# Performance work log

Hardware: AMD Instinct MI355X
Metric: run time of the kernel (lower is better)

Reference implementation:

```python
import jax, jax.numpy as jnp
import numpy as np

NUM_LINKS = 4096
BUDGET = 100.0      # total_power_budget
PMAX = 0.1          # per_link_max
N_BISECT = 60       # bisection iterations (fp32 converges well before this)


def setup_inputs() -> dict:
    key = jax.random.key(0)
    raw_power = jax.random.normal(key, (8192, NUM_LINKS), dtype=jnp.float32)
    return {"raw_power": raw_power}


def _project(raw):
    """Euclidean projection of each row of raw onto {p : 0<=p<=PMAX, sum(p)<=BUDGET}.

    Closed-form water-filling: if clip(raw,0,PMAX) is feasible it is the answer;
    otherwise p = clip(raw - tau, 0, PMAX) with tau chosen so sum(p) = BUDGET
    (found by batched bisection + one implicit-function Newton correction,
    which also gives the exact QP-projection Jacobian).
    """
    clipped = jnp.clip(raw, 0.0, PMAX)
    feasible = jnp.sum(clipped, axis=-1, keepdims=True) <= BUDGET  # (B,1)

    raw_sg = jax.lax.stop_gradient(raw)
    lo = jnp.min(raw_sg, axis=-1, keepdims=True) - PMAX  # g(lo) = n*PMAX >= BUDGET
    hi = jnp.max(raw_sg, axis=-1, keepdims=True)         # g(hi) = 0

    def body(_, lohi):
        lo, hi = lohi
        mid = 0.5 * (lo + hi)
        g = jnp.sum(jnp.clip(raw_sg - mid, 0.0, PMAX), axis=-1, keepdims=True)
        too_big = g > BUDGET  # tau must increase
        return (jnp.where(too_big, mid, lo), jnp.where(too_big, hi, mid))

    lo, hi = jax.lax.fori_loop(0, N_BISECT, body, (lo, hi))
    tau0 = 0.5 * (lo + hi)  # (B,1), no gradient

    # Implicit-function (Newton) correction: g(tau) = sum(clip(raw-tau,0,PMAX)) = BUDGET.
    # dg/dtau = -n_active, dg/draw_i = active_i  => dtau/draw_i = active_i / n_active.
    active = (raw_sg - tau0 > 0.0) & (raw_sg - tau0 < PMAX)
    n_active = jnp.maximum(jnp.sum(active, axis=-1, keepdims=True).astype(raw.dtype), 1.0)
    g0 = jnp.sum(jnp.clip(raw - tau0, 0.0, PMAX), axis=-1, keepdims=True)
    tau = tau0 + (g0 - BUDGET) / n_active  # value ~= tau0, correct gradient

    p_budget = jnp.clip(raw - tau, 0.0, PMAX)
    return jnp.where(feasible, clipped, p_budget)


def reference(raw_power) -> jnp.ndarray:
    return _project(raw_power)
```

## Files before the change

kernel.cpp:

```cpp
#include <hip/hip_runtime.h>

#define NLINKS 4096
#define VEC 16

constexpr float kPmax = 0.1f;
constexpr float kBudget = 100.0f;
constexpr int kBisect = 20;

__device__ __forceinline__ float waveReduceSum(float x) {
#pragma unroll
  for (int m = 32; m >= 1; m >>= 1) x += __shfl_xor(x, m, 64);
  return x;
}
__device__ __forceinline__ float waveReduceMin(float x) {
#pragma unroll
  for (int m = 32; m >= 1; m >>= 1) x = fminf(x, __shfl_xor(x, m, 64));
  return x;
}
__device__ __forceinline__ float waveReduceMax(float x) {
#pragma unroll
  for (int m = 32; m >= 1; m >>= 1) x = fmaxf(x, __shfl_xor(x, m, 64));
  return x;
}

__device__ __forceinline__ float clip01(float x) {
  return fminf(fmaxf(x, 0.0f), kPmax);
}

__global__ __launch_bounds__(256, 4) void proj_kernel(
    const float* __restrict__ raw, float* __restrict__ out, int rows) {
  const int wave = threadIdx.x >> 6;
  const int lane = threadIdx.x & 63;
  const int row = blockIdx.x * 4 + wave;
  if (row >= rows) return;

  const float4* rp = (const float4*)(raw + (size_t)row * NLINKS);
  float4* op = (float4*)(out + (size_t)row * NLINKS);

  float4 v[VEC];
#pragma unroll
  for (int j = 0; j < VEC; ++j) v[j] = rp[lane + 64 * j];

  float mn = 1e30f, mx = -1e30f;
  float fs0 = 0.f, fs1 = 0.f, fs2 = 0.f, fs3 = 0.f;
#pragma unroll
  for (int j = 0; j < VEC; ++j) {
    mn = fminf(mn, fminf(fminf(v[j].x, v[j].y), fminf(v[j].z, v[j].w)));
    mx = fmaxf(mx, fmaxf(fmaxf(v[j].x, v[j].y), fmaxf(v[j].z, v[j].w)));
    fs0 += clip01(v[j].x);
    fs1 += clip01(v[j].y);
    fs2 += clip01(v[j].z);
    fs3 += clip01(v[j].w);
  }
  const float fs = waveReduceSum((fs0 + fs1) + (fs2 + fs3));
  mn = waveReduceMin(mn);
  mx = waveReduceMax(mx);

  if (fs <= kBudget) {
#pragma unroll
    for (int j = 0; j < VEC; ++j) {
      float4 o;
      o.x = clip01(v[j].x);
      o.y = clip01(v[j].y);
      o.z = clip01(v[j].z);
      o.w = clip01(v[j].w);
      op[lane + 64 * j] = o;
    }
    return;
  }

  float lo = mn - kPmax, hi = mx;
#pragma unroll 1
  for (int it = 0; it < kBisect; ++it) {
    const float mid = 0.5f * (lo + hi);
    float s0 = 0.f, s1 = 0.f, s2 = 0.f, s3 = 0.f;
#pragma unroll
    for (int j = 0; j < VEC; ++j) {
      s0 += clip01(v[j].x - mid);
      s1 += clip01(v[j].y - mid);
      s2 += clip01(v[j].z - mid);
      s3 += clip01(v[j].w - mid);
    }
    const float g = waveReduceSum((s0 + s1) + (s2 + s3));
    const bool big = g > kBudget;
    lo = big ? mid : lo;
    hi = big ? hi : mid;
  }
  const float tau0 = 0.5f * (lo + hi);

  float g0 = 0.f, g1 = 0.f, g2 = 0.f, g3 = 0.f;
  float n0 = 0.f, n1 = 0.f, n2 = 0.f, n3 = 0.f;
#pragma unroll
  for (int j = 0; j < VEC; ++j) {
    float t;
    t = v[j].x - tau0; g0 += clip01(t); n0 += (t > 0.f && t < kPmax) ? 1.f : 0.f;
    t = v[j].y - tau0; g1 += clip01(t); n1 += (t > 0.f && t < kPmax) ? 1.f : 0.f;
    t = v[j].z - tau0; g2 += clip01(t); n2 += (t > 0.f && t < kPmax) ? 1.f : 0.f;
    t = v[j].w - tau0; g3 += clip01(t); n3 += (t > 0.f && t < kPmax) ? 1.f : 0.f;
  }
  const float g = waveReduceSum((g0 + g1) + (g2 + g3));
  float na = waveReduceSum((n0 + n1) + (n2 + n3));
  na = fmaxf(na, 1.0f);
  const float tau = tau0 + (g - kBudget) / na;

#pragma unroll
  for (int j = 0; j < VEC; ++j) {
    float4 o;
    o.x = clip01(v[j].x - tau);
    o.y = clip01(v[j].y - tau);
    o.z = clip01(v[j].z - tau);
    o.w = clip01(v[j].w - tau);
    op[lane + 64 * j] = o;
  }
}

extern "C" void kernel_launch(void* const* d_in, const int* in_sizes, int n_in,
                              void* d_out, int out_size, void* d_ws, size_t ws_size,
                              hipStream_t stream) {
  const float* raw = (const float*)d_in[0];
  float* out = (float*)d_out;
  const int rows = in_sizes[0] / NLINKS;
  const int blocks = (rows + 3) / 4;
  hipLaunchKernelGGL(proj_kernel, dim3(blocks), dim3(256), 0, stream,
                     raw, out, rows);
}
```

Before: 264.0 us.

## Replace bisection with Illinois regula falsi root finder and nontemporal memory ops

Swaps the 20-step bisection for the threshold tau with a 10-step Illinois-style regula falsi bracketed on [0, max], dropping the row-min reduction. Clipping now uses the fmed3 builtin, and the loads and stores go through nontemporal builtins. This halves the number of per-row sweeps over registers and wave reductions. The risk is slower or less accurate convergence for some rows, which the final Newton correction may not fully repair.

```diff
diff --git a/kernel.cpp b/kernel.cpp
--- a/kernel.cpp
+++ b/kernel.cpp
@@ -3,18 +3,15 @@
 #define NLINKS 4096
 #define VEC 16
 
+typedef float fvec4 __attribute__((ext_vector_type(4)));
+
 constexpr float kPmax = 0.1f;
 constexpr float kBudget = 100.0f;
-constexpr int kBisect = 20;
+constexpr int kSecant = 10;
 
 __device__ __forceinline__ float waveReduceSum(float x) {
 #pragma unroll
   for (int m = 32; m >= 1; m >>= 1) x += __shfl_xor(x, m, 64);
-  return x;
-}
-__device__ __forceinline__ float waveReduceMin(float x) {
-#pragma unroll
-  for (int m = 32; m >= 1; m >>= 1) x = fminf(x, __shfl_xor(x, m, 64));
   return x;
 }
 __device__ __forceinline__ float waveReduceMax(float x) {
@@ -24,7 +21,7 @@
 }
 
 __device__ __forceinline__ float clip01(float x) {
-  return fminf(fmaxf(x, 0.0f), kPmax);
+  return __builtin_amdgcn_fmed3f(x, 0.0f, kPmax);
 }
 
 __global__ __launch_bounds__(256, 4) void proj_kernel(
@@ -34,18 +31,17 @@
   const int row = blockIdx.x * 4 + wave;
   if (row >= rows) return;
 
-  const float4* rp = (const float4*)(raw + (size_t)row * NLINKS);
-  float4* op = (float4*)(out + (size_t)row * NLINKS);
+  const fvec4* rp = (const fvec4*)(raw + (size_t)row * NLINKS);
+  fvec4* op = (fvec4*)(out + (size_t)row * NLINKS);
 
-  float4 v[VEC];
+  fvec4 v[VEC];
 #pragma unroll
-  for (int j = 0; j < VEC; ++j) v[j] = rp[lane + 64 * j];
+  for (int j = 0; j < VEC; ++j) v[j] = __builtin_nontemporal_load(&rp[lane + 64 * j]);
 
-  float mn = 1e30f, mx = -1e30f;
+  float mx = -1e30f;
   float fs0 = 0.f, fs1 = 0.f, fs2 = 0.f, fs3 = 0.f;
 #pragma unroll
   for (int j = 0; j < VEC; ++j) {
-    mn = fminf(mn, fminf(fminf(v[j].x, v[j].y), fminf(v[j].z, v[j].w)));
     mx = fmaxf(mx, fmaxf(fmaxf(v[j].x, v[j].y), fmaxf(v[j].z, v[j].w)));
     fs0 += clip01(v[j].x);
     fs1 += clip01(v[j].y);
@@ -53,40 +49,53 @@
     fs3 += clip01(v[j].w);
   }
   const float fs = waveReduceSum((fs0 + fs1) + (fs2 + fs3));
-  mn = waveReduceMin(mn);
   mx = waveReduceMax(mx);
 
   if (fs <= kBudget) {
 #pragma unroll
     for (int j = 0; j < VEC; ++j) {
-      float4 o;
+      fvec4 o;
       o.x = clip01(v[j].x);
       o.y = clip01(v[j].y);
       o.z = clip01(v[j].z);
       o.w = clip01(v[j].w);
-      op[lane + 64 * j] = o;
+      __builtin_nontemporal_store(o, &op[lane + 64 * j]);
     }
     return;
   }
 
-  float lo = mn - kPmax, hi = mx;
+  float a = 0.f, ga = fs;
+  float b = mx, gb = 0.f;
+  int side = 0;
 #pragma unroll 1
-  for (int it = 0; it < kBisect; ++it) {
-    const float mid = 0.5f * (lo + hi);
+  for (int it = 0; it < kSecant; ++it) {
+    const float denom = gb - ga;
+    float t = b - (gb - kBudget) * (b - a) / denom;
+    if (!(t > a && t < b)) t = 0.5f * (a + b);
+
     float s0 = 0.f, s1 = 0.f, s2 = 0.f, s3 = 0.f;
 #pragma unroll
     for (int j = 0; j < VEC; ++j) {
-      s0 += clip01(v[j].x - mid);
-      s1 += clip01(v[j].y - mid);
-      s2 += clip01(v[j].z - mid);
-      s3 += clip01(v[j].w - mid);
+      s0 += clip01(v[j].x - t);
+      s1 += clip01(v[j].y - t);
+      s2 += clip01(v[j].z - t);
+      s3 += clip01(v[j].w - t);
     }
     const float g = waveReduceSum((s0 + s1) + (s2 + s3));
-    const bool big = g > kBudget;
-    lo = big ? mid : lo;
-    hi = big ? hi : mid;
+
+    if (g > kBudget) {
+      a = t; ga = g;
+      if (side == 1) gb = kBudget + 0.5f * (gb - kBudget);
+      side = 1;
+    } else {
+      b = t; gb = g;
+      if (side == -1) ga = kBudget + 0.5f * (ga - kBudget);
+      side = -1;
+    }
   }
-  const float tau0 = 0.5f * (lo + hi);
+  const float dd = gb - ga;
+  float tau0 = (dd != 0.f) ? b - (gb - kBudget) * (b - a) / dd : 0.5f * (a + b);
+  if (!(tau0 >= a && tau0 <= b)) tau0 = 0.5f * (a + b);
 
   float g0 = 0.f, g1 = 0.f, g2 = 0.f, g3 = 0.f;
   float n0 = 0.f, n1 = 0.f, n2 = 0.f, n3 = 0.f;
@@ -105,12 +114,12 @@
 
 #pragma unroll
   for (int j = 0; j < VEC; ++j) {
-    float4 o;
+    fvec4 o;
     o.x = clip01(v[j].x - tau);
     o.y = clip01(v[j].y - tau);
     o.z = clip01(v[j].z - tau);
     o.w = clip01(v[j].w - tau);
-    op[lane + 64 * j] = o;
+    __builtin_nontemporal_store(o, &op[lane + 64 * j]);
   }
 }
 
```

After: 261.6 us. No clear change (-0.9%).
